# Kernel optimization log

Hardware: AMD Instinct MI355X
Metric: run time of the kernel (lower is better)

## Reference

```python
import jax, jax.numpy as jnp
import numpy as np
from jax import lax

STRIDE = 4
SCALES = (32.0, 64.0, 128.0)
RATIOS = (0.5, 1.0, 2.0)
PRE_NMS = 6000          # pre_nms_top_n['testing']
POST_NMS = 1000         # post_nms_top_n['testing']
NMS_THRESH = 0.7
MIN_SIZE = 1.0


def make_anchors(fh, fw):
    # 9 base anchors per cell (3 scales x 3 ratios), xyxy centered at cell centers.
    base = []
    for s in SCALES:
        for r in RATIOS:
            w = s * np.sqrt(1.0 / r)
            h = s * np.sqrt(r)
            base.append([-w / 2, -h / 2, w / 2, h / 2])
    base = np.asarray(base, np.float32)                      # [9,4]
    xs = (np.arange(fw, dtype=np.float32) + 0.5) * STRIDE
    ys = (np.arange(fh, dtype=np.float32) + 0.5) * STRIDE
    cx, cy = np.meshgrid(xs, ys)                             # [fh,fw]
    shifts = np.stack([cx, cy, cx, cy], -1)[:, :, None, :]   # [fh,fw,1,4]
    return jnp.asarray((shifts + base[None, None]).reshape(-1, 4))  # [fh*fw*9,4]


def conv(x, w, b):
    y = lax.conv_general_dilated(x, w, (1, 1), 'SAME',
                                 dimension_numbers=('NCHW', 'OIHW', 'NCHW'))
    return y + b[None, :, None, None]


def decode(anchors, deltas):
    wa = anchors[:, 2] - anchors[:, 0]
    ha = anchors[:, 3] - anchors[:, 1]
    cxa = anchors[:, 0] + 0.5 * wa
    cya = anchors[:, 1] + 0.5 * ha
    cx = deltas[:, 0] * wa + cxa
    cy = deltas[:, 1] * ha + cya
    w = jnp.exp(deltas[:, 2]) * wa
    h = jnp.exp(deltas[:, 3]) * ha
    return jnp.stack([cx - 0.5 * w, cy - 0.5 * h, cx + 0.5 * w, cy + 0.5 * h], -1)


def pairwise_iou(a, b):
    area_a = (a[:, 2] - a[:, 0]) * (a[:, 3] - a[:, 1])
    area_b = (b[:, 2] - b[:, 0]) * (b[:, 3] - b[:, 1])
    lt = jnp.maximum(a[:, None, :2], b[None, :, :2])
    rb = jnp.minimum(a[:, None, 2:], b[None, :, 2:])
    wh = jnp.clip(rb - lt, 0.0)
    inter = wh[..., 0] * wh[..., 1]
    return inter / (area_a[:, None] + area_b[None, :] - inter + 1e-9)


def nms_keep(boxes, valid, thresh):
    # boxes already sorted by score descending; greedy suppression.
    n = boxes.shape[0]
    iou = pairwise_iou(boxes, boxes)  # [n,n]
    def body(i, keep):
        suppressed = jnp.any((iou[i] > thresh) & keep)
        return keep.at[i].set(valid[i] & ~suppressed)
    return lax.fori_loop(0, n, body, jnp.zeros(n, bool))


def rpn_forward(feature, w1, b1, w_cls, b_cls, w_reg, b_reg, image_h, image_w,
                detach_for_proposal=True):
    fh, fw = feature.shape[2], feature.shape[3]
    x = jax.nn.relu(conv(feature, w1, b1))
    conf = conv(x, w_cls, b_cls).transpose(0, 2, 3, 1).reshape(-1)        # [N]
    offsets = conv(x, w_reg, b_reg).transpose(0, 2, 3, 1).reshape(-1, 4)  # [N,4]
    if detach_for_proposal:  # original detaches before create_proposal
        conf = lax.stop_gradient(conf)
        offsets = lax.stop_gradient(offsets)
    anchors = make_anchors(fh, fw)

    pre_n = min(PRE_NMS, conf.shape[0])
    scores, idx = lax.top_k(conf, pre_n)
    props = decode(anchors[idx], offsets[idx])
    # process_box: clip to image, drop boxes smaller than min_size (mask form)
    props = jnp.stack([jnp.clip(props[:, 0], 0.0, float(image_w)),
                       jnp.clip(props[:, 1], 0.0, float(image_h)),
                       jnp.clip(props[:, 2], 0.0, float(image_w)),
                       jnp.clip(props[:, 3], 0.0, float(image_h))], -1)
    valid = ((props[:, 2] - props[:, 0]) >= MIN_SIZE) & \
            ((props[:, 3] - props[:, 1]) >= MIN_SIZE)

    keep = nms_keep(lax.stop_gradient(props), valid, NMS_THRESH)
    # compact first POST_NMS kept boxes into a fixed-shape output (zero padded)
    rank = jnp.cumsum(keep) - 1
    dest = jnp.where(keep & (rank < POST_NMS), rank, POST_NMS)
    out = jnp.zeros((POST_NMS + 1, 4), props.dtype).at[dest].set(props)[:POST_NMS]
    return out


def setup_inputs() -> dict:
    key = jax.random.key(0)
    ks = jax.random.split(key, 4)
    return {
        'feature': jax.random.normal(ks[0], (1, 256, 200, 272), jnp.float32),
        'w1': jax.random.normal(ks[1], (256, 256, 3, 3), jnp.float32) * 0.02,
        'b1': jnp.zeros((256,), jnp.float32),
        'w_cls': jax.random.normal(ks[2], (9, 256, 1, 1), jnp.float32) * 0.02,
        'b_cls': jnp.zeros((9,), jnp.float32),
        'w_reg': jax.random.normal(ks[3], (36, 256, 1, 1), jnp.float32) * 0.01,
        'b_reg': jnp.zeros((36,), jnp.float32),
        'image_h': 800,
        'image_w': 1088,
    }


def reference(feature, w1, b1, w_cls, b_cls, w_reg, b_reg, image_h, image_w):
    return rpn_forward(feature, w1, b1, w_cls, b_cls, w_reg, b_reg,
                       image_h, image_w, detach_for_proposal=True)
```

## Files before the change

kernel.cpp:

```cpp
#include <hip/hip_runtime.h>
#include <hip/hip_bf16.h>
#include <math.h>

#define H_ 200
#define W_ 272
#define C_ 256
#define HW 54400
#define NANCH 489600
#define PRE_N 6000
#define POST_N 1000
#define NWORDS 94
#define CHUNK_W 2720
#define SELCAP 16384

#define X_OFF       0ull
#define CONF_OFF    55705600ull
#define HIST1_OFF   57664000ull
#define SEL_OFF     57926144ull
#define SCAL_OFF    58188288ull
#define TOPIDX_OFF  58254080ull
#define BOXES_OFF   58278080ull
#define VALID_OFF   58374080ull
#define MASK_OFF    58398080ull
#define WCR_OFF     65269376ull

__device__ __forceinline__ unsigned fkey(float fv) {
    unsigned u = __float_as_uint(fv);
    return (u & 0x80000000u) ? ~u : (u | 0x80000000u);
}

__global__ __launch_bounds__(256) void k_conv1(const float* __restrict__ f,
                                               const float* __restrict__ w1,
                                               const float* __restrict__ b1,
                                               float* __restrict__ xo,
                                               unsigned* __restrict__ hist1,
                                               unsigned* __restrict__ scal,
                                               unsigned long long* __restrict__ sel,
                                               const float* __restrict__ wcls,
                                               float* __restrict__ wcr) {
    __shared__ __align__(16) float sI[2][2880];
    int tid = threadIdx.x;
    int fb = blockIdx.x + 9 * (blockIdx.y + 25 * blockIdx.z);
    {
        int g = fb * 256 + tid;
        if (g < 65536) hist1[g] = 0u;
        else if (g < 65600) scal[g - 65536] = 0u;
        else if (g < 98368) ((unsigned*)sel)[g - 65600] = 0xFFFFFFFFu;
    }
    if (fb == 0) {
        for (int e = tid; e < 2304; e += 256) {
            int a = e / 256, c = e % 256;
            wcr[c * 9 + a] = wcls[e];
        }
    }
    int lane = tid & 63;
    int wgl = __builtin_amdgcn_readfirstlane(tid >> 6);
    int xg = lane & 7;
    int yg = lane >> 3;
    int X0 = blockIdx.x * 32;
    int Y0 = blockIdx.y * 8;
    int wg = blockIdx.z * 4 + wgl;
    int y = Y0 + yg;
    int xbase = X0 + xg * 4;

    int off[11]; int lds[11]; bool ok[11];
#pragma unroll
    for (int it = 0; it < 11; it++) {
        int l = tid + it * 256;
        int ci = l / 340; int r = l - ci * 340; int ry = r / 34; int rx = r - ry * 34;
        int gx = X0 - 1 + rx, gy = Y0 - 1 + ry;
        ok[it] = (l < CHUNK_W) && gx >= 0 && gx < W_ && gy >= 0 && gy < H_;
        off[it] = ci * HW + gy * W_ + gx;
        lds[it] = (ci * 10 + ry) * 36 + rx;
    }
    float rbuf[11];
#pragma unroll
    for (int it = 0; it < 11; it++)
        rbuf[it] = ok[it] ? f[off[it]] : 0.f;
#pragma unroll
    for (int it = 0; it < 11; it++)
        if (tid + it * 256 < CHUNK_W) sI[0][lds[it]] = rbuf[it];
    __syncthreads();

    float acc[8][4];
#pragma unroll
    for (int o = 0; o < 8; o++)
#pragma unroll
        for (int i = 0; i < 4; i++) acc[o][i] = 0.f;

    const float* wbase = w1 + (size_t)(wg * 8) * 2304;

    int cur = 0;
    for (int ic0 = 0; ic0 < 256; ic0 += 8) {
        if (ic0 < 248) {
            const float* fn = f + (size_t)(ic0 + 8) * HW;
#pragma unroll
            for (int it = 0; it < 11; it++)
                rbuf[it] = ok[it] ? fn[off[it]] : 0.f;
        }
        const float* sbuf = sI[cur];
        for (int ci = 0; ci < 8; ci++) {
            const float* wci = wbase + (ic0 + ci) * 9;
#pragma unroll
            for (int ky = 0; ky < 3; ky++) {
                const float* irow = &sbuf[(ci * 10 + yg + ky) * 36 + xg * 4];
                float4 va = *(const float4*)irow;
                float2 vb = *(const float2*)(irow + 4);
                float in[6] = {va.x, va.y, va.z, va.w, vb.x, vb.y};
#pragma unroll
                for (int kx = 0; kx < 3; kx++) {
#pragma unroll
                    for (int o = 0; o < 8; o++) {
                        float w = wci[o * 2304 + ky * 3 + kx];
#pragma unroll
                        for (int i = 0; i < 4; i++)
                            acc[o][i] = fmaf(w, in[i + kx], acc[o][i]);
                    }
                }
            }
        }
        if (ic0 < 248) {
#pragma unroll
            for (int it = 0; it < 11; it++)
                if (tid + it * 256 < CHUNK_W) sI[cur ^ 1][lds[it]] = rbuf[it];
        }
        __syncthreads();
        cur ^= 1;
    }
#pragma unroll
    for (int o = 0; o < 8; o++) {
        int oc = wg * 8 + o;
        float bv = b1[oc];
        float* orow = xo + (size_t)oc * HW + y * W_ + xbase;
        float v0 = fmaxf(acc[o][0] + bv, 0.f), v1 = fmaxf(acc[o][1] + bv, 0.f);
        float v2 = fmaxf(acc[o][2] + bv, 0.f), v3 = fmaxf(acc[o][3] + bv, 0.f);
        if (xbase + 3 < W_) {
            *(float4*)orow = make_float4(v0, v1, v2, v3);
        } else {
            float vv[4] = {v0, v1, v2, v3};
            for (int i = 0; i < 4; i++)
                if (xbase + i < W_) orow[i] = vv[i];
        }
    }
}

__global__ __launch_bounds__(256) void k_cls(const float* __restrict__ x,
                                             const float* __restrict__ wcr,
                                             const float* __restrict__ bc,
                                             float* __restrict__ conf,
                                             unsigned* __restrict__ hist) {
    int p = blockIdx.x * 256 + threadIdx.x;
    if (p >= HW) return;
    float acc[9];
#pragma unroll
    for (int a = 0; a < 9; a++) acc[a] = 0.f;
    for (int c = 0; c < 256; c++) {
        float xv = x[c * HW + p];
        const float* wp = wcr + c * 9;
#pragma unroll
        for (int a = 0; a < 9; a++) acc[a] = fmaf(wp[a], xv, acc[a]);
    }
#pragma unroll
    for (int a = 0; a < 9; a++) {
        float v = acc[a] + bc[a];
        conf[p * 9 + a] = v;
        atomicAdd(&hist[fkey(v) >> 16], 1u);
    }
}

__global__ __launch_bounds__(1024) void k_scan(const unsigned* __restrict__ hist,
                                               unsigned* scal) {
    __shared__ unsigned ssum[1024];
    int t = threadIdx.x;
    int base = 65535 - t * 64;
    unsigned s = 0;
    {
        const uint4* hp = (const uint4*)(hist + (base - 63));
#pragma unroll
        for (int k = 0; k < 16; k++) { uint4 v = hp[k]; s += v.x + v.y + v.z + v.w; }
    }
    ssum[t] = s;
    __syncthreads();
    for (int off = 1; off < 1024; off <<= 1) {
        unsigned v = (t >= off) ? ssum[t - off] : 0u;
        __syncthreads();
        ssum[t] += v;
        __syncthreads();
    }
    unsigned incl = ssum[t], excl = incl - s;
    if (excl < 6000u && 6000u <= incl) {
        unsigned run = excl;
        bool found = false;
        for (int pass = 0; pass < 2 && !found; pass++) {
            unsigned c32[32];
#pragma unroll
            for (int j = 0; j < 32; j++) c32[j] = hist[base - (pass * 32 + j)];
            for (int j = 0; j < 32; j++) {
                if (run + c32[j] >= 6000u) {
                    scal[0] = (unsigned)(base - (pass * 32 + j));
                    scal[1] = run;
                    found = true;
                    break;
                }
                run += c32[j];
            }
        }
    }
}

__global__ __launch_bounds__(256) void k_gather(const float* __restrict__ conf,
                                                unsigned* scal, unsigned long long* sel) {
    int n = blockIdx.x * 256 + threadIdx.x;
    if (n >= NANCH) return;
    unsigned B1 = scal[0], cnt1 = scal[1];
    unsigned key = fkey(conf[n]);
    unsigned pre = key >> 16;
    if (pre < B1) return;
    unsigned long long kk = ((unsigned long long)(~key) << 32) | (unsigned)n;
    if (pre > B1) {
        unsigned pos = atomicAdd(&scal[4], 1u);
        sel[pos] = kk;
    } else {
        unsigned pos = cnt1 + atomicAdd(&scal[5], 1u);
        if (pos < SELCAP) sel[pos] = kk;
    }
}

__global__ __launch_bounds__(256) void k_rank(const unsigned* __restrict__ scal,
                                              const unsigned long long* __restrict__ sel,
                                              unsigned* __restrict__ topidx) {
    __shared__ unsigned long long tile[2048];
    unsigned filled = scal[1] + scal[5];
    if (filled > SELCAP) filled = SELCAP;
    int i = blockIdx.x * 256 + threadIdx.x;
    unsigned long long mykey = sel[i];
    int rank = 0;
    for (int t0 = 0; t0 < SELCAP; t0 += 2048) {
        if (t0 >= (int)filled) break;
        __syncthreads();
        for (int l = threadIdx.x; l < 2048; l += 256)
            tile[l] = sel[t0 + l];
        __syncthreads();
        for (int l = 0; l < 2048; l += 4) {
            ulonglong2 p = *(const ulonglong2*)&tile[l];
            ulonglong2 q = *(const ulonglong2*)&tile[l + 2];
            rank += (p.x < mykey) + (p.y < mykey) + (q.x < mykey) + (q.y < mykey);
        }
    }
    if (i < (int)filled && rank < PRE_N)
        topidx[rank] = (unsigned)(mykey & 0xFFFFFFFFull);
}

__global__ __launch_bounds__(64) void k_prop(const float* __restrict__ x,
                                             const float* __restrict__ wreg,
                                             const float* __restrict__ breg,
                                             const unsigned* __restrict__ topidx,
                                             const int* __restrict__ imh, const int* __restrict__ imw,
                                             float* __restrict__ boxes, int* __restrict__ valid) {
    int r = blockIdx.x;
    int lane = threadIdx.x;
    unsigned n = topidx[r];
    int a = (int)(n % 9u); int p = (int)(n / 9u);
    const float* wr = wreg + (4 * a) * 256;
    float s0 = 0, s1 = 0, s2 = 0, s3 = 0;
    for (int c = lane; c < 256; c += 64) {
        float xv = x[c * HW + p];
        s0 = fmaf(wr[c], xv, s0);
        s1 = fmaf(wr[256 + c], xv, s1);
        s2 = fmaf(wr[512 + c], xv, s2);
        s3 = fmaf(wr[768 + c], xv, s3);
    }
#pragma unroll
    for (int off = 32; off >= 1; off >>= 1) {
        s0 += __shfl_down(s0, off);
        s1 += __shfl_down(s1, off);
        s2 += __shfl_down(s2, off);
        s3 += __shfl_down(s3, off);
    }
    if (lane == 0) {
        float dx = s0 + breg[4 * a], dy = s1 + breg[4 * a + 1];
        float dw = s2 + breg[4 * a + 2], dh = s3 + breg[4 * a + 3];
        int wi = p % W_, hi = p / W_;
        const double SC[3] = {32.0, 64.0, 128.0};
        const double RT[3] = {0.5, 1.0, 2.0};
        double sd = SC[a / 3], rd = RT[a % 3];
        double wb = sd * sqrt(1.0 / rd), hb = sd * sqrt(rd);
        float bx1 = (float)(-wb * 0.5), by1 = (float)(-hb * 0.5);
        float bx2 = (float)(wb * 0.5),  by2 = (float)(hb * 0.5);
        float cxs = ((float)wi + 0.5f) * 4.0f, cys = ((float)hi + 0.5f) * 4.0f;
        float x1a = cxs + bx1, y1a = cys + by1, x2a = cxs + bx2, y2a = cys + by2;
        float wa = x2a - x1a, ha = y2a - y1a;
        float cxa = x1a + 0.5f * wa, cya = y1a + 0.5f * ha;
        float cx = dx * wa + cxa, cy = dy * ha + cya;
        float ww = expf(dw) * wa, hh = expf(dh) * ha;
        float X1 = cx - 0.5f * ww, Y1 = cy - 0.5f * hh;
        float X2 = cx + 0.5f * ww, Y2 = cy + 0.5f * hh;
        float Wf = (float)(*imw), Hf = (float)(*imh);
        X1 = fminf(fmaxf(X1, 0.f), Wf); Y1 = fminf(fmaxf(Y1, 0.f), Hf);
        X2 = fminf(fmaxf(X2, 0.f), Wf); Y2 = fminf(fmaxf(Y2, 0.f), Hf);
        boxes[4 * r] = X1; boxes[4 * r + 1] = Y1; boxes[4 * r + 2] = X2; boxes[4 * r + 3] = Y2;
        valid[r] = ((X2 - X1) >= 1.0f && (Y2 - Y1) >= 1.0f) ? 1 : 0;
    }
}

__global__ __launch_bounds__(256) void k_mask(const float* __restrict__ boxes,
                                              unsigned long long* __restrict__ mask) {
    __shared__ float jb[256];
    int jw = blockIdx.x;
    int i = blockIdx.y * 256 + threadIdx.x;
    {
        int idx = jw * 256 + threadIdx.x;
        jb[threadIdx.x] = (idx < PRE_N * 4) ? boxes[idx] : 0.f;
    }
    __syncthreads();
    if (i >= PRE_N) return;
    float ax1 = boxes[4 * i], ay1 = boxes[4 * i + 1], ax2 = boxes[4 * i + 2], ay2 = boxes[4 * i + 3];
    float aarea = (ax2 - ax1) * (ay2 - ay1);
    unsigned long long m = 0;
    int jbase = jw * 64;
    for (int b = 0; b < 64; b++) {
        int j = jbase + b;
        if (j <= i || j >= PRE_N) continue;
        float bx1 = jb[4 * b], by1 = jb[4 * b + 1], bx2 = jb[4 * b + 2], by2 = jb[4 * b + 3];
        float barea = (bx2 - bx1) * (by2 - by1);
        float xx1 = fmaxf(ax1, bx1), yy1 = fmaxf(ay1, by1);
        float xx2 = fminf(ax2, bx2), yy2 = fminf(ay2, by2);
        float w = fmaxf(xx2 - xx1, 0.f), h = fmaxf(yy2 - yy1, 0.f);
        float inter = w * h;
        float iou = inter / (aarea + barea - inter + 1e-9f);
        if (iou > 0.7f) m |= (1ull << b);
    }
    mask[(size_t)i * NWORDS + jw] = m;
}

__global__ __launch_bounds__(128) void k_scan_nms(const unsigned long long* __restrict__ mask,
                                                  const int* __restrict__ valid,
                                                  const float* __restrict__ boxes,
                                                  float* __restrict__ out) {
    __shared__ unsigned long long diag[NWORDS][64];
    __shared__ unsigned long long removed[NWORDS];
    __shared__ unsigned long long validw[NWORDS];
    __shared__ int keepList[POST_N];
    __shared__ int cnt;
    __shared__ unsigned long long keptbits;
    int t = threadIdx.x;
    if (t < NWORDS) { removed[t] = 0ull; validw[t] = 0ull; }
    if (t == 0) cnt = 0;
    __syncthreads();
    for (int l = t; l < NWORDS * 64; l += 128) {
        int w = l >> 6, b = l & 63;
        int i = w * 64 + b;
        diag[w][b] = (i < PRE_N) ? mask[(size_t)i * NWORDS + w] : 0ull;
    }
    for (int i = t; i < PRE_N; i += 128)
        if (valid[i]) atomicOr(&validw[i >> 6], 1ull << (i & 63));
    __syncthreads();
    for (int w = 0; w < NWORDS; w++) {
        unsigned long long candw = validw[w] & ~removed[w];
        if (!candw) continue;
        if (t == 0) {
            unsigned long long cand = candw;
            unsigned long long kb = 0ull;
            int c = cnt;
            while (cand && c < POST_N) {
                int b = __ffsll((unsigned long long)cand) - 1;
                keepList[c++] = w * 64 + b;
                kb |= 1ull << b;
                cand &= ~(1ull << b);
                cand &= ~diag[w][b];
            }
            cnt = c; keptbits = kb;
        }
        __syncthreads();
        if (cnt >= POST_N) break;
        unsigned long long kb = keptbits;
        if (kb) {
            for (int w2 = w + 1 + t; w2 < NWORDS; w2 += 128) {
                unsigned long long acc2 = removed[w2];
                unsigned long long tt = kb;
                while (tt) {
                    int b = __ffsll((unsigned long long)tt) - 1;
                    tt &= tt - 1;
                    acc2 |= mask[(size_t)(w * 64 + b) * NWORDS + w2];
                }
                removed[w2] = acc2;
            }
        }
        __syncthreads();
    }
    __syncthreads();
    int c = cnt;
    for (int e = t; e < POST_N * 4; e += 128) {
        int r = e >> 2;
        out[e] = (r < c) ? boxes[4 * keepList[r] + (e & 3)] : 0.f;
    }
}

extern "C" void kernel_launch(void* const* d_in, const int* in_sizes, int n_in,
                              void* d_out, int out_size, void* d_ws, size_t ws_size,
                              hipStream_t stream) {
    const float* feature = (const float*)d_in[0];
    const float* w1   = (const float*)d_in[1];
    const float* b1   = (const float*)d_in[2];
    const float* wcls = (const float*)d_in[3];
    const float* bcls = (const float*)d_in[4];
    const float* wreg = (const float*)d_in[5];
    const float* breg = (const float*)d_in[6];
    const int* imh = (const int*)d_in[7];
    const int* imw = (const int*)d_in[8];

    char* ws = (char*)d_ws;
    float* xbuf  = (float*)(ws + X_OFF);
    float* conf  = (float*)(ws + CONF_OFF);
    unsigned* hist1 = (unsigned*)(ws + HIST1_OFF);
    unsigned* scal  = (unsigned*)(ws + SCAL_OFF);
    unsigned long long* sel = (unsigned long long*)(ws + SEL_OFF);
    unsigned* topidx = (unsigned*)(ws + TOPIDX_OFF);
    float* boxes = (float*)(ws + BOXES_OFF);
    int* valid   = (int*)(ws + VALID_OFF);
    unsigned long long* mask = (unsigned long long*)(ws + MASK_OFF);
    float* wcr = (float*)(ws + WCR_OFF);
    float* outF = (float*)d_out;

    hipLaunchKernelGGL(k_conv1,  dim3(9, 25, 8), dim3(256), 0, stream,
                       feature, w1, b1, xbuf, hist1, scal, sel, wcls, wcr);
    hipLaunchKernelGGL(k_cls,    dim3(213),  dim3(256), 0, stream, xbuf, wcr, bcls, conf, hist1);
    hipLaunchKernelGGL(k_scan,   dim3(1),    dim3(1024), 0, stream, hist1, scal);
    hipLaunchKernelGGL(k_gather, dim3(1913), dim3(256), 0, stream, conf, scal, sel);
    hipLaunchKernelGGL(k_rank,   dim3(64),   dim3(256), 0, stream, scal, sel, topidx);
    hipLaunchKernelGGL(k_prop,   dim3(PRE_N), dim3(64), 0, stream, xbuf, wreg, breg, topidx, imh, imw, boxes, valid);
    hipLaunchKernelGGL(k_mask,   dim3(NWORDS, 24), dim3(256), 0, stream, boxes, mask);
    hipLaunchKernelGGL(k_scan_nms, dim3(1), dim3(128), 0, stream, mask, valid, boxes, outF);
}
```

Before: 1.545 ms.

## Retile conv1 to 16 output channels by 2 pixels with repacked weights

Adds a weight repack kernel that lays out w1 as [group16][ic][tap][16 oc], so each thread's 16 output-channel weights for a tap are contiguous, uniform scalar loads. The conv tile shrinks to 16x8 pixels, with each thread computing 2 pixels for 16 output channels and a launch grid of 17x25x4. The aim is better weight reuse per input load and a smaller LDS footprint, which may raise occupancy. The trade-offs are a larger halo overhead from the narrower tile, reuse of the mask workspace area to hold the repacked weights, and an extra launch.

New measurement: 1.619 ms. 4.8% more time.

```diff
diff --git a/kernel.cpp b/kernel.cpp
--- a/kernel.cpp
+++ b/kernel.cpp
@@ -10,7 +10,7 @@
 #define PRE_N 6000
 #define POST_N 1000
 #define NWORDS 94
-#define CHUNK_W 2720
+#define CHUNK_W 1440
 #define SELCAP 16384
 
 #define X_OFF       0ull
@@ -29,8 +29,19 @@
     return (u & 0x80000000u) ? ~u : (u | 0x80000000u);
 }
 
+__global__ __launch_bounds__(256) void k_repack(const float* __restrict__ w1,
+                                                float* __restrict__ w1r) {
+    int d = blockIdx.x * 256 + threadIdx.x;
+    int o = d & 15;
+    int q = d >> 4;
+    int t = q % 9;
+    int icg = q / 9;
+    int wg16 = icg >> 8, ic = icg & 255;
+    w1r[d] = w1[((size_t)(wg16 * 16 + o) * 256 + ic) * 9 + t];
+}
+
 __global__ __launch_bounds__(256) void k_conv1(const float* __restrict__ f,
-                                               const float* __restrict__ w1,
+                                               const float* __restrict__ w1r,
                                                const float* __restrict__ b1,
                                                float* __restrict__ xo,
                                                unsigned* __restrict__ hist1,
@@ -38,9 +49,9 @@
                                                unsigned long long* __restrict__ sel,
                                                const float* __restrict__ wcls,
                                                float* __restrict__ wcr) {
-    __shared__ __align__(16) float sI[2][2880];
+    __shared__ __align__(16) float sI[2][1600];
     int tid = threadIdx.x;
-    int fb = blockIdx.x + 9 * (blockIdx.y + 25 * blockIdx.z);
+    int fb = blockIdx.x + 17 * (blockIdx.y + 25 * blockIdx.z);
     {
         int g = fb * 256 + tid;
         if (g < 65536) hist1[g] = 0u;
@@ -57,90 +68,81 @@
     int wgl = __builtin_amdgcn_readfirstlane(tid >> 6);
     int xg = lane & 7;
     int yg = lane >> 3;
-    int X0 = blockIdx.x * 32;
+    int X0 = blockIdx.x * 16;
     int Y0 = blockIdx.y * 8;
-    int wg = blockIdx.z * 4 + wgl;
+    int wg16 = blockIdx.z * 4 + wgl;
     int y = Y0 + yg;
-    int xbase = X0 + xg * 4;
-
-    int off[11]; int lds[11]; bool ok[11];
-#pragma unroll
-    for (int it = 0; it < 11; it++) {
+    int xbase = X0 + xg * 2;
+
+    int off[6]; int lds[6]; bool ok[6];
+#pragma unroll
+    for (int it = 0; it < 6; it++) {
         int l = tid + it * 256;
-        int ci = l / 340; int r = l - ci * 340; int ry = r / 34; int rx = r - ry * 34;
+        int ci = l / 180; int r = l - ci * 180; int ry = r / 18; int rx = r - ry * 18;
         int gx = X0 - 1 + rx, gy = Y0 - 1 + ry;
         ok[it] = (l < CHUNK_W) && gx >= 0 && gx < W_ && gy >= 0 && gy < H_;
         off[it] = ci * HW + gy * W_ + gx;
-        lds[it] = (ci * 10 + ry) * 36 + rx;
-    }
-    float rbuf[11];
-#pragma unroll
-    for (int it = 0; it < 11; it++)
+        lds[it] = (ci * 10 + ry) * 20 + rx;
+    }
+    float rbuf[6];
+#pragma unroll
+    for (int it = 0; it < 6; it++)
         rbuf[it] = ok[it] ? f[off[it]] : 0.f;
 #pragma unroll
-    for (int it = 0; it < 11; it++)
+    for (int it = 0; it < 6; it++)
         if (tid + it * 256 < CHUNK_W) sI[0][lds[it]] = rbuf[it];
     __syncthreads();
 
-    float acc[8][4];
-#pragma unroll
-    for (int o = 0; o < 8; o++)
-#pragma unroll
-        for (int i = 0; i < 4; i++) acc[o][i] = 0.f;
-
-    const float* wbase = w1 + (size_t)(wg * 8) * 2304;
+    float acc[16][2];
+#pragma unroll
+    for (int o = 0; o < 16; o++) { acc[o][0] = 0.f; acc[o][1] = 0.f; }
+
+    const float* wbase = w1r + (size_t)wg16 * (256 * 144);
 
     int cur = 0;
     for (int ic0 = 0; ic0 < 256; ic0 += 8) {
         if (ic0 < 248) {
             const float* fn = f + (size_t)(ic0 + 8) * HW;
 #pragma unroll
-            for (int it = 0; it < 11; it++)
+            for (int it = 0; it < 6; it++)
                 rbuf[it] = ok[it] ? fn[off[it]] : 0.f;
         }
         const float* sbuf = sI[cur];
         for (int ci = 0; ci < 8; ci++) {
-            const float* wci = wbase + (ic0 + ci) * 9;
+            const float* wci = wbase + (ic0 + ci) * 144;
 #pragma unroll
             for (int ky = 0; ky < 3; ky++) {
-                const float* irow = &sbuf[(ci * 10 + yg + ky) * 36 + xg * 4];
-                float4 va = *(const float4*)irow;
-                float2 vb = *(const float2*)(irow + 4);
-                float in[6] = {va.x, va.y, va.z, va.w, vb.x, vb.y};
+                const float* irow = &sbuf[(ci * 10 + yg + ky) * 20 + xg * 2];
+                float2 pa = *(const float2*)irow;
+                float2 pb = *(const float2*)(irow + 2);
+                float in[4] = {pa.x, pa.y, pb.x, pb.y};
 #pragma unroll
                 for (int kx = 0; kx < 3; kx++) {
-#pragma unroll
-                    for (int o = 0; o < 8; o++) {
-                        float w = wci[o * 2304 + ky * 3 + kx];
-#pragma unroll
-                        for (int i = 0; i < 4; i++)
-                            acc[o][i] = fmaf(w, in[i + kx], acc[o][i]);
+                    const float* w16 = wci + (ky * 3 + kx) * 16;
+#pragma unroll
+                    for (int o = 0; o < 16; o++) {
+                        float w = w16[o];
+                        acc[o][0] = fmaf(w, in[kx], acc[o][0]);
+                        acc[o][1] = fmaf(w, in[kx + 1], acc[o][1]);
                     }
                 }
             }
         }
         if (ic0 < 248) {
 #pragma unroll
-            for (int it = 0; it < 11; it++)
+            for (int it = 0; it < 6; it++)
                 if (tid + it * 256 < CHUNK_W) sI[cur ^ 1][lds[it]] = rbuf[it];
         }
         __syncthreads();
         cur ^= 1;
     }
 #pragma unroll
-    for (int o = 0; o < 8; o++) {
-        int oc = wg * 8 + o;
+    for (int o = 0; o < 16; o++) {
+        int oc = wg16 * 16 + o;
         float bv = b1[oc];
         float* orow = xo + (size_t)oc * HW + y * W_ + xbase;
         float v0 = fmaxf(acc[o][0] + bv, 0.f), v1 = fmaxf(acc[o][1] + bv, 0.f);
-        float v2 = fmaxf(acc[o][2] + bv, 0.f), v3 = fmaxf(acc[o][3] + bv, 0.f);
-        if (xbase + 3 < W_) {
-            *(float4*)orow = make_float4(v0, v1, v2, v3);
-        } else {
-            float vv[4] = {v0, v1, v2, v3};
-            for (int i = 0; i < 4; i++)
-                if (xbase + i < W_) orow[i] = vv[i];
-        }
+        *(float2*)orow = make_float2(v0, v1);
     }
 }
 
@@ -419,11 +421,13 @@
     float* boxes = (float*)(ws + BOXES_OFF);
     int* valid   = (int*)(ws + VALID_OFF);
     unsigned long long* mask = (unsigned long long*)(ws + MASK_OFF);
+    float* w1r = (float*)(ws + MASK_OFF);
     float* wcr = (float*)(ws + WCR_OFF);
     float* outF = (float*)d_out;
 
-    hipLaunchKernelGGL(k_conv1,  dim3(9, 25, 8), dim3(256), 0, stream,
-                       feature, w1, b1, xbuf, hist1, scal, sel, wcls, wcr);
+    hipLaunchKernelGGL(k_repack, dim3(2304), dim3(256), 0, stream, w1, w1r);
+    hipLaunchKernelGGL(k_conv1,  dim3(17, 25, 4), dim3(256), 0, stream,
+                       feature, w1r, b1, xbuf, hist1, scal, sel, wcls, wcr);
     hipLaunchKernelGGL(k_cls,    dim3(213),  dim3(256), 0, stream, xbuf, wcr, bcls, conf, hist1);
     hipLaunchKernelGGL(k_scan,   dim3(1),    dim3(1024), 0, stream, hist1, scal);
     hipLaunchKernelGGL(k_gather, dim3(1913), dim3(256), 0, stream, conf, scal, sel);
```
